# Performance work log

Hardware: AMD Instinct MI355X
Metric: run time of the kernel (lower is better)

The kernel has to match this reference:

```python
import jax, jax.numpy as jnp
import numpy as np

DILATED = (1, 2, 3)
NUM_PROTOS = 100
PROTO_SIZE = 4
ENC_SIZE = 1600
NUM_CLASSES = 2
B, L = 64, 256

# num_filters split exactly as in torch: floor(P/len) each, first gets remainder
_nf = [NUM_PROTOS // len(DILATED)] * len(DILATED)
_nf[0] += NUM_PROTOS % len(DILATED)
NUM_FILTERS = tuple(_nf)  # (34, 33, 33)


def setup_inputs() -> dict:
    key = jax.random.key(0)
    k1, k2, k3 = jax.random.split(key, 3)
    embedding = jax.random.normal(k1, (B, L, ENC_SIZE), dtype=jnp.float32)
    # nn.init.uniform_ default is U[0,1)
    protolayer = jax.random.uniform(k2, (NUM_PROTOS, ENC_SIZE, PROTO_SIZE), dtype=jnp.float32)
    fc_w = jax.random.normal(k3, (NUM_CLASSES, NUM_PROTOS), dtype=jnp.float32) * 0.1
    return {"embedding": embedding, "protolayer": protolayer, "fc_w": fc_w}


def _l2_convolution(x_bel, protolayer):
    # x_bel: [B, L, E] -> [B, E, L] for NCH conv layout
    x = jnp.transpose(x_bel, (0, 2, 1))
    # sliding-window sum of x^2 computed ONCE per dilation (shared across protos,
    # mathematically identical to conv1d with all-ones weight)
    s = jnp.sum(x * x, axis=1)  # [B, L]
    p2_sum = jnp.sum(protolayer * protolayer, axis=(1, 2))  # [P]
    distances = []
    j = 0
    Lx = x.shape[2]
    for d, n in zip(DILATED, NUM_FILTERS):
        L_out = Lx - (PROTO_SIZE - 1) * d
        # windowed sum over K=PROTO_SIZE taps with dilation d: [B, L_out]
        x2_patch = sum(s[:, k * d:k * d + L_out] for k in range(PROTO_SIZE))
        # dilated cross-correlation x * p : [B, n, L_out]
        xp = jax.lax.conv_general_dilated(
            x, protolayer[j:j + n],
            window_strides=(1,), padding='VALID', rhs_dilation=(d,),
            dimension_numbers=('NCH', 'OIH', 'NCH'))
        dist = jnp.sqrt(jnp.abs(x2_patch[:, None, :] - 2.0 * xp
                                + p2_sum[j:j + n][None, :, None]))
        distances.append(dist)
        j += n
    return distances


def reference(embedding, protolayer, fc_w):
    distances = _l2_convolution(embedding, protolayer)
    prototype_distances = jnp.concatenate(
        [jnp.min(d, axis=2) for d in distances], axis=1)  # [B, P]
    class_out = prototype_distances @ fc_w.T  # [B, num_classes]
    return (prototype_distances, distances[0], distances[1], distances[2], class_out)
```

## Files before the change

kernel.cpp:

```cpp
#include <hip/hip_runtime.h>

#define B_   64
#define L_   256
#define E_   1600
#define P_   100
#define KP   4
#define N0 34
#define N1 33
#define N2 33
#define LOUT0 253
#define LOUT1 250
#define LOUT2 247
#define OFF_PD 0
#define OFF_D0 6400
#define OFF_D1 (OFF_D0 + B_*N0*LOUT0)
#define OFF_D2 (OFF_D1 + B_*N1*LOUT1)
#define OFF_CO (OFF_D2 + B_*N2*LOUT2)

#define WS_ABF  0ull
#define WS_BT   52428800ull
#define WS_S    (WS_BT + 1280000ull)
#define WS_P2   (WS_S + 65536ull)
#define WS_NEED (WS_P2 + 512ull)

#define TMF  96
#define BKB  128
#define BOFF2 12288

typedef float f32x4 __attribute__((ext_vector_type(4)));
typedef unsigned short ushort8v __attribute__((ext_vector_type(8)));
typedef __bf16 bf16x8 __attribute__((ext_vector_type(8)));
typedef _Float16 f16;

__device__ __forceinline__ unsigned short bf16rne(float f) {
    unsigned u = __float_as_uint(f);
    u += 0x7FFFu + ((u >> 16) & 1u);
    return (unsigned short)(u >> 16);
}

typedef __attribute__((address_space(3))) void lds_void_t;
typedef __attribute__((address_space(1))) void glb_void_t;

__device__ __forceinline__ void gload16(const void* g, void* l) {
    __builtin_amdgcn_global_load_lds((const glb_void_t*)g, (lds_void_t*)l, 16, 0, 0);
}


__global__ __launch_bounds__(256) void proto_prep_fast(
        const float* __restrict__ emb, const float* __restrict__ proto,
        char* __restrict__ ws, float* __restrict__ out) {
    int q = blockIdx.x;
    int wave = threadIdx.x >> 6, lane = threadIdx.x & 63;
    if (q < 4096) {
        int row = q * 4 + wave;
        const float4* r = (const float4*)(emb + (size_t)row * E_);
        unsigned short* dst = (unsigned short*)(ws + WS_ABF + (size_t)row * (E_*2));
        float acc = 0.f;
        #pragma unroll
        for (int it = 0; it < 6; ++it) {
            int e4 = it * 64 + lane;
            float4 v = r[e4];
            acc += v.x*v.x + v.y*v.y + v.z*v.z + v.w*v.w;
            ushort4 bv = make_ushort4(bf16rne(v.x), bf16rne(v.y),
                                      bf16rne(v.z), bf16rne(v.w));
            *(ushort4*)(dst + e4 * 4) = bv;
        }
        if (lane < 16) {
            int e4 = 384 + lane;
            float4 v = r[e4];
            acc += v.x*v.x + v.y*v.y + v.z*v.z + v.w*v.w;
            ushort4 bv = make_ushort4(bf16rne(v.x), bf16rne(v.y),
                                      bf16rne(v.z), bf16rne(v.w));
            *(ushort4*)(dst + e4 * 4) = bv;
        }
        #pragma unroll
        for (int off = 32; off; off >>= 1) acc += __shfl_down(acc, off);
        if (lane == 0) ((float*)(ws + WS_S))[row] = acc;
    } else if (q < 4121) {
        int p = (q - 4096) * 4 + wave;
        if (p < P_) {
            const float4* r = (const float4*)(proto + (size_t)p * (E_ * KP));
            unsigned short* bt = (unsigned short*)(ws + WS_BT);
            float acc = 0.f;
            #pragma unroll
            for (int it = 0; it < 25; ++it) {
                int e = it * 64 + lane;
                float4 v = r[e];
                acc += v.x*v.x + v.y*v.y + v.z*v.z + v.w*v.w;
                bt[(size_t)(4*p + 0) * E_ + e] = bf16rne(v.x);
                bt[(size_t)(4*p + 1) * E_ + e] = bf16rne(v.y);
                bt[(size_t)(4*p + 2) * E_ + e] = bf16rne(v.z);
                bt[(size_t)(4*p + 3) * E_ + e] = bf16rne(v.w);
            }
            #pragma unroll
            for (int off = 32; off; off >>= 1) acc += __shfl_down(acc, off);
            if (lane == 0) ((float*)(ws + WS_P2))[p] = acc;
        }
    } else {
        for (int i = threadIdx.x; i < B_ * P_; i += 256)
            out[OFF_PD + i] = __uint_as_float(0x7F800000u);
    }
}

__global__ __launch_bounds__(192, 4) void proto_main_fast(
        const char* __restrict__ ws, float* __restrict__ out) {

    __shared__ __align__(16) char smem[22528];

    int bx   = blockIdx.x;
    int lb   = (bx & 7) * 120 + (bx >> 3);
    int b     = lb / 15;
    int inner = lb % 15;
    int m     = inner / 5;
    int n_blk = inner % 5;
    int r0    = (m == 0) ? 0 : (m == 1 ? 87 : 160);
    int l_lo  = m * 87;
    int pbase = n_blk * 20;

    const char* Ag = ws + WS_ABF + (size_t)(b * L_ + r0) * (E_ * 2);
    const char* Bg = ws + WS_BT  + (size_t)(pbase * 4) * (E_ * 2);

    int tid   = threadIdx.x;
    int lane  = tid & 63;
    int wave  = tid >> 6;
    int mrow  = lane & 15;
    int jq    = lane >> 4;
    int lrow8 = lane >> 3;
    int jst   = lane & 7;

    f32x4 acc[2][5] = {};

    for (int c = 0; c < 25; ++c) {
        int eoff = c * BKB;
        for (int t = wave; t < 22; t += 3) {
            if (t < 12) {
                int rowl = t * 8 + lrow8;
                int j = jst ^ (rowl & 7);
                gload16(Ag + (size_t)rowl * (E_*2) + eoff + j * 16,
                        smem + t * 1024);
            } else {
                int rowl = (t - 12) * 8 + lrow8;
                int j = jst ^ (rowl & 7);
                gload16(Bg + (size_t)rowl * (E_*2) + eoff + j * 16,
                        smem + BOFF2 + (t - 12) * 1024);
            }
        }
        __syncthreads();

        #pragma unroll
        for (int ks = 0; ks < 2; ++ks) {
            ushort8v af[2];
            #pragma unroll
            for (int mi = 0; mi < 2; ++mi) {
                int rowA = wave * 32 + mi * 16 + mrow;
                af[mi] = *(const ushort8v*)(smem + rowA * 128
                            + (((ks << 2) + jq) ^ (rowA & 7)) * 16);
            }
            ushort8v bfv[5];
            #pragma unroll
            for (int ni = 0; ni < 5; ++ni) {
                int rowB = ni * 16 + mrow;
                bfv[ni] = *(const ushort8v*)(smem + BOFF2 + rowB * 128
                            + (((ks << 2) + jq) ^ (rowB & 7)) * 16);
            }
            #pragma unroll
            for (int mi = 0; mi < 2; ++mi)
                #pragma unroll
                for (int ni = 0; ni < 5; ++ni)
                    acc[mi][ni] = __builtin_amdgcn_mfma_f32_16x16x32_bf16(
                        __builtin_bit_cast(bf16x8, af[mi]),
                        __builtin_bit_cast(bf16x8, bfv[ni]),
                        acc[mi][ni], 0, 0, 0);
        }
        __syncthreads();
    }

    f16*      Yh     = (f16*)smem;
    float*    slds   = (float*)(smem + 15552);
    float*    p2lds  = slds + TMF;
    unsigned* minlds = (unsigned*)(p2lds + 20);

    {
        int colq = lane & 15;
        int rowq = (lane >> 4) * 4;
        #pragma unroll
        for (int mi = 0; mi < 2; ++mi) {
            int row = wave * 32 + mi * 16 + rowq;
            #pragma unroll
            for (int ni = 0; ni < 5; ++ni) {
                int col = ni * 16 + colq;
                #pragma unroll
                for (int r = 0; r < 4; ++r)
                    Yh[(row + r) * 81 + col] = (f16)acc[mi][ni][r];
            }
        }
    }
    if (tid < TMF) slds[tid] = ((const float*)(ws + WS_S))[b * L_ + r0 + tid];
    if (tid < 20) {
        p2lds[tid] = ((const float*)(ws + WS_P2))[pbase + tid];
        minlds[tid] = 0x7F800000u;
    }
    __syncthreads();

    for (int idx = tid; idx < 20 * 87; idx += 192) {
        int pl  = idx / 87;
        int lof = idx % 87;
        int p = pbase + pl;
        int d, Lout, nseg, pseg; size_t segbase;
        if (p < 34)      { d = 1; Lout = LOUT0; segbase = OFF_D0; pseg = p;      nseg = N0; }
        else if (p < 67) { d = 2; Lout = LOUT1; segbase = OFF_D1; pseg = p - 34; nseg = N1; }
        else             { d = 3; Lout = LOUT2; segbase = OFF_D2; pseg = p - 67; nseg = N2; }
        int l = l_lo + lof;
        if (l < Lout) {
            int rl = l - r0;
            int c0 = pl * 4;
            float xp = (float)Yh[rl * 81 + c0]
                     + (float)Yh[(rl + d) * 81 + c0 + 1]
                     + (float)Yh[(rl + 2*d) * 81 + c0 + 2]
                     + (float)Yh[(rl + 3*d) * 81 + c0 + 3];
            float x2 = slds[rl] + slds[rl + d] + slds[rl + 2*d] + slds[rl + 3*d];
            float dist = sqrtf(fabsf(x2 - 2.f * xp + p2lds[pl]));
            out[segbase + ((size_t)b * nseg + pseg) * Lout + l] = dist;
            atomicMin(&minlds[pl], __float_as_uint(dist));
        }
    }
    __syncthreads();
    if (tid < 20)
        atomicMin((unsigned*)out + OFF_PD + b * P_ + pbase + tid, minlds[tid]);
}

#define TM   144
#define ASTR 40
#define YSTR 81

__global__ __launch_bounds__(256) void proto_prep_kernel(
        const float* __restrict__ emb, const float* __restrict__ proto,
        float* __restrict__ ws_s, float* __restrict__ ws_p2,
        float* __restrict__ out) {
    int q = blockIdx.x;
    int wave = threadIdx.x >> 6, lane = threadIdx.x & 63;
    if (q < 4096) {
        int row = q * 4 + wave;
        const float4* r = (const float4*)(emb + (size_t)row * E_);
        float acc = 0.f;
        #pragma unroll
        for (int it = 0; it < 7; ++it) {
            int e4 = it * 64 + lane;
            if (e4 < 400) {
                float4 v = r[e4];
                acc += v.x*v.x + v.y*v.y + v.z*v.z + v.w*v.w;
            }
        }
        #pragma unroll
        for (int off = 32; off; off >>= 1) acc += __shfl_down(acc, off);
        if (lane == 0) ws_s[row] = acc;
    } else if (q < 4121) {
        int p = (q - 4096) * 4 + wave;
        if (p < P_) {
            const float4* r = (const float4*)(proto + (size_t)p * (E_ * KP));
            float acc = 0.f;
            #pragma unroll
            for (int it = 0; it < 25; ++it) {
                float4 v = r[it * 64 + lane];
                acc += v.x*v.x + v.y*v.y + v.z*v.z + v.w*v.w;
            }
            #pragma unroll
            for (int off = 32; off; off >>= 1) acc += __shfl_down(acc, off);
            if (lane == 0) ws_p2[p] = acc;
        }
    } else {
        for (int i = threadIdx.x; i < B_ * P_; i += 256)
            out[OFF_PD + i] = __uint_as_float(0x7F800000u);
    }
}

__global__ __launch_bounds__(192) void proto_main_kernel(
        const float* __restrict__ emb, const float* __restrict__ proto,
        const float* __restrict__ ws_s, const float* __restrict__ ws_p2,
        float* __restrict__ out) {

    __shared__ __align__(16) char smem[47392];
    unsigned short* Ald = (unsigned short*)smem;
    unsigned short* Bld = (unsigned short*)(smem + TM*ASTR*2);

    int bx = blockIdx.x;
    int n_blk = bx % 5;
    int m     = (bx / 5) & 1;
    int b     = bx / 10;
    int r0    = m ? 112 : 0;
    int pbase = n_blk * 20;

    const float* Abase = emb + ((size_t)(b * L_ + r0)) * E_;
    const float* Bbase = proto + (size_t)pbase * (E_ * KP);

    int tid  = threadIdx.x;
    int lane = tid & 63;
    int wave = tid >> 6;
    int mrow = lane & 15;
    int kq   = (lane >> 4) * 8;

    f32x4 acc[3][5] = {};

    for (int c = 0; c < E_ / 32; ++c) {
        int e0 = c * 32;
        #pragma unroll
        for (int i = 0; i < 6; ++i) {
            int idx = tid + i * 192;
            int row = idx >> 3;
            int e4  = idx & 7;
            float4 v = *(const float4*)(Abase + (size_t)row * E_ + e0 + e4 * 4);
            ushort4 bv = make_ushort4(bf16rne(v.x), bf16rne(v.y),
                                      bf16rne(v.z), bf16rne(v.w));
            *(ushort4*)&Ald[row * ASTR + e4 * 4] = bv;
        }
        for (int idx = tid; idx < 640; idx += 192) {
            int pl = idx >> 5;
            int el = idx & 31;
            float4 v = *(const float4*)(Bbase + (size_t)pl * (E_ * KP)
                                        + (size_t)(e0 + el) * KP);
            Bld[(4*pl + 0) * ASTR + el] = bf16rne(v.x);
            Bld[(4*pl + 1) * ASTR + el] = bf16rne(v.y);
            Bld[(4*pl + 2) * ASTR + el] = bf16rne(v.z);
            Bld[(4*pl + 3) * ASTR + el] = bf16rne(v.w);
        }
        __syncthreads();

        ushort8v af[3], bfr[5];
        #pragma unroll
        for (int mi = 0; mi < 3; ++mi)
            af[mi] = *(const ushort8v*)&Ald[(wave*48 + mi*16 + mrow) * ASTR + kq];
        #pragma unroll
        for (int ni = 0; ni < 5; ++ni)
            bfr[ni] = *(const ushort8v*)&Bld[(ni*16 + mrow) * ASTR + kq];
        #pragma unroll
        for (int mi = 0; mi < 3; ++mi)
            #pragma unroll
            for (int ni = 0; ni < 5; ++ni)
                acc[mi][ni] = __builtin_amdgcn_mfma_f32_16x16x32_bf16(
                    __builtin_bit_cast(bf16x8, af[mi]),
                    __builtin_bit_cast(bf16x8, bfr[ni]),
                    acc[mi][ni], 0, 0, 0);
        __syncthreads();
    }

    float*    Ylds   = (float*)smem;
    float*    slds   = (float*)(smem + TM * YSTR * 4);
    float*    p2lds  = slds + TM;
    unsigned* minlds = (unsigned*)(p2lds + 20);

    {
        int colq = lane & 15;
        int rowq = (lane >> 4) * 4;
        #pragma unroll
        for (int mi = 0; mi < 3; ++mi) {
            int row = wave * 48 + mi * 16 + rowq;
            #pragma unroll
            for (int ni = 0; ni < 5; ++ni) {
                int col = ni * 16 + colq;
                #pragma unroll
                for (int r = 0; r < 4; ++r)
                    Ylds[(row + r) * YSTR + col] = acc[mi][ni][r];
            }
        }
    }
    if (tid < TM) slds[tid] = ws_s[b * L_ + r0 + tid];
    if (tid < 20) { p2lds[tid] = ws_p2[pbase + tid]; minlds[tid] = 0x7F800000u; }
    __syncthreads();

    int l_lo = m * 128;
    for (int idx = tid; idx < 20 * 128; idx += 192) {
        int pl  = idx >> 7;
        int lof = idx & 127;
        int p = pbase + pl;
        int d, Lout, nseg, pseg; size_t segbase;
        if (p < 34)      { d = 1; Lout = LOUT0; segbase = OFF_D0; pseg = p;      nseg = N0; }
        else if (p < 67) { d = 2; Lout = LOUT1; segbase = OFF_D1; pseg = p - 34; nseg = N1; }
        else             { d = 3; Lout = LOUT2; segbase = OFF_D2; pseg = p - 67; nseg = N2; }
        int l = l_lo + lof;
        if (l < Lout) {
            int rl = l - r0;
            int c0 = pl * 4;
            float xp = Ylds[rl * YSTR + c0]
                     + Ylds[(rl + d) * YSTR + c0 + 1]
                     + Ylds[(rl + 2*d) * YSTR + c0 + 2]
                     + Ylds[(rl + 3*d) * YSTR + c0 + 3];
            float x2 = slds[rl] + slds[rl + d] + slds[rl + 2*d] + slds[rl + 3*d];
            float dist = sqrtf(fabsf(x2 - 2.f * xp + p2lds[pl]));
            out[segbase + ((size_t)b * nseg + pseg) * Lout + l] = dist;
            atomicMin(&minlds[pl], __float_as_uint(dist));
        }
    }
    __syncthreads();
    if (tid < 20)
        atomicMin((unsigned*)out + OFF_PD + b * P_ + pbase + tid, minlds[tid]);
}

__global__ __launch_bounds__(128) void proto_fc_kernel(
        const float* __restrict__ fc_w, float* __restrict__ out) {
    int t = threadIdx.x;
    int b = t >> 1, c = t & 1;
    const float* pd = out + OFF_PD + b * P_;
    const float* w  = fc_w + c * P_;
    float s = 0.f;
    #pragma unroll 4
    for (int p = 0; p < P_; ++p) s += pd[p] * w[p];
    out[OFF_CO + b * 2 + c] = s;
}

extern "C" void kernel_launch(void* const* d_in, const int* in_sizes, int n_in,
                              void* d_out, int out_size, void* d_ws, size_t ws_size,
                              hipStream_t stream) {
    const float* emb   = (const float*)d_in[0];
    const float* proto = (const float*)d_in[1];
    const float* fc_w  = (const float*)d_in[2];
    float* out  = (float*)d_out;

    if (ws_size >= WS_NEED) {
        char* ws = (char*)d_ws;
        proto_prep_fast<<<4122, 256, 0, stream>>>(emb, proto, ws, out);
        proto_main_fast<<<960, 192, 0, stream>>>(ws, out);
    } else {
        float* ws_s  = (float*)d_ws;
        float* ws_p2 = ws_s + B_ * L_;
        proto_prep_kernel<<<4122, 256, 0, stream>>>(emb, proto, ws_s, ws_p2, out);
        proto_main_kernel<<<640, 192, 0, stream>>>(emb, proto, ws_s, ws_p2, out);
    }
    proto_fc_kernel<<<1, 128, 0, stream>>>(fc_w, out);
}
```

Measured before the change: 215.6 us.

## Fuse embedding bf16 conversion and squared-norm into main GEMM kernel

After: 236.0 us. +9.5%, slower.

```diff
diff --git a/kernel.cpp b/kernel.cpp
--- a/kernel.cpp
+++ b/kernel.cpp
@@ -17,14 +17,11 @@
 #define OFF_D2 (OFF_D1 + B_*N1*LOUT1)
 #define OFF_CO (OFF_D2 + B_*N2*LOUT2)
 
-#define WS_ABF  0ull
-#define WS_BT   52428800ull
-#define WS_S    (WS_BT + 1280000ull)
-#define WS_P2   (WS_S + 65536ull)
+#define WS_BT   0ull
+#define WS_P2   1280000ull
 #define WS_NEED (WS_P2 + 512ull)
 
 #define TMF  96
-#define BKB  128
 #define BOFF2 12288
 
 typedef float f32x4 __attribute__((ext_vector_type(4)));
@@ -46,64 +43,38 @@
 }
 
 
-__global__ __launch_bounds__(256) void proto_prep_fast(
-        const float* __restrict__ emb, const float* __restrict__ proto,
-        char* __restrict__ ws, float* __restrict__ out) {
+__global__ __launch_bounds__(256) void proto_prepB_fast(
+        const float* __restrict__ proto, char* __restrict__ ws,
+        float* __restrict__ out) {
     int q = blockIdx.x;
     int wave = threadIdx.x >> 6, lane = threadIdx.x & 63;
-    if (q < 4096) {
-        int row = q * 4 + wave;
-        const float4* r = (const float4*)(emb + (size_t)row * E_);
-        unsigned short* dst = (unsigned short*)(ws + WS_ABF + (size_t)row * (E_*2));
+    if (q < 25) {
+        int p = q * 4 + wave;
+        const float4* r = (const float4*)(proto + (size_t)p * (E_ * KP));
+        unsigned short* bt = (unsigned short*)(ws + WS_BT);
         float acc = 0.f;
         #pragma unroll
-        for (int it = 0; it < 6; ++it) {
-            int e4 = it * 64 + lane;
-            float4 v = r[e4];
+        for (int it = 0; it < 25; ++it) {
+            int e = it * 64 + lane;
+            float4 v = r[e];
             acc += v.x*v.x + v.y*v.y + v.z*v.z + v.w*v.w;
-            ushort4 bv = make_ushort4(bf16rne(v.x), bf16rne(v.y),
-                                      bf16rne(v.z), bf16rne(v.w));
-            *(ushort4*)(dst + e4 * 4) = bv;
-        }
-        if (lane < 16) {
-            int e4 = 384 + lane;
-            float4 v = r[e4];
-            acc += v.x*v.x + v.y*v.y + v.z*v.z + v.w*v.w;
-            ushort4 bv = make_ushort4(bf16rne(v.x), bf16rne(v.y),
-                                      bf16rne(v.z), bf16rne(v.w));
-            *(ushort4*)(dst + e4 * 4) = bv;
+            bt[(size_t)(4*p + 0) * E_ + e] = bf16rne(v.x);
+            bt[(size_t)(4*p + 1) * E_ + e] = bf16rne(v.y);
+            bt[(size_t)(4*p + 2) * E_ + e] = bf16rne(v.z);
+            bt[(size_t)(4*p + 3) * E_ + e] = bf16rne(v.w);
         }
         #pragma unroll
         for (int off = 32; off; off >>= 1) acc += __shfl_down(acc, off);
-        if (lane == 0) ((float*)(ws + WS_S))[row] = acc;
-    } else if (q < 4121) {
-        int p = (q - 4096) * 4 + wave;
-        if (p < P_) {
-            const float4* r = (const float4*)(proto + (size_t)p * (E_ * KP));
-            unsigned short* bt = (unsigned short*)(ws + WS_BT);
-            float acc = 0.f;
-            #pragma unroll
-            for (int it = 0; it < 25; ++it) {
-                int e = it * 64 + lane;
-                float4 v = r[e];
-                acc += v.x*v.x + v.y*v.y + v.z*v.z + v.w*v.w;
-                bt[(size_t)(4*p + 0) * E_ + e] = bf16rne(v.x);
-                bt[(size_t)(4*p + 1) * E_ + e] = bf16rne(v.y);
-                bt[(size_t)(4*p + 2) * E_ + e] = bf16rne(v.z);
-                bt[(size_t)(4*p + 3) * E_ + e] = bf16rne(v.w);
-            }
-            #pragma unroll
-            for (int off = 32; off; off >>= 1) acc += __shfl_down(acc, off);
-            if (lane == 0) ((float*)(ws + WS_P2))[p] = acc;
-        }
+        if (lane == 0) ((float*)(ws + WS_P2))[p] = acc;
     } else {
         for (int i = threadIdx.x; i < B_ * P_; i += 256)
             out[OFF_PD + i] = __uint_as_float(0x7F800000u);
     }
 }
 
-__global__ __launch_bounds__(192, 4) void proto_main_fast(
-        const char* __restrict__ ws, float* __restrict__ out) {
+__global__ __launch_bounds__(192, 3) void proto_main_fused(
+        const float* __restrict__ emb, const char* __restrict__ ws,
+        float* __restrict__ out) {
 
     __shared__ __align__(16) char smem[22528];
 
@@ -117,8 +88,8 @@
     int l_lo  = m * 87;
     int pbase = n_blk * 20;
 
-    const char* Ag = ws + WS_ABF + (size_t)(b * L_ + r0) * (E_ * 2);
-    const char* Bg = ws + WS_BT  + (size_t)(pbase * 4) * (E_ * 2);
+    const char* Ag = (const char*)emb + (size_t)(b * L_ + r0) * (E_ * 4);
+    const char* Bg = ws + WS_BT + (size_t)(pbase * 4) * (E_ * 2);
 
     int tid   = threadIdx.x;
     int lane  = tid & 63;
@@ -127,23 +98,38 @@
     int jq    = lane >> 4;
     int lrow8 = lane >> 3;
     int jst   = lane & 7;
+    int g8    = (tid >> 4) * 8;
+    int kk    = tid & 15;
 
     f32x4 acc[2][5] = {};
+    float sacc[8] = {};
 
     for (int c = 0; c < 25; ++c) {
-        int eoff = c * BKB;
-        for (int t = wave; t < 22; t += 3) {
-            if (t < 12) {
-                int rowl = t * 8 + lrow8;
-                int j = jst ^ (rowl & 7);
-                gload16(Ag + (size_t)rowl * (E_*2) + eoff + j * 16,
-                        smem + t * 1024);
-            } else {
-                int rowl = (t - 12) * 8 + lrow8;
-                int j = jst ^ (rowl & 7);
-                gload16(Bg + (size_t)rowl * (E_*2) + eoff + j * 16,
-                        smem + BOFF2 + (t - 12) * 1024);
-            }
+        int eoffB = c * 128;
+        int eoffA = c * 256;
+
+        for (int t = wave; t < 10; t += 3) {
+            int rowl = t * 8 + lrow8;
+            int j = jst ^ (rowl & 7);
+            gload16(Bg + (size_t)rowl * (E_*2) + eoffB + j * 16,
+                    smem + BOFF2 + t * 1024);
+        }
+
+        float4 va[8];
+        #pragma unroll
+        for (int i = 0; i < 8; ++i) {
+            int row = g8 + i;
+            va[i] = *(const float4*)(Ag + (size_t)row * (E_*4) + eoffA + kk * 16);
+        }
+        #pragma unroll
+        for (int i = 0; i < 8; ++i) {
+            int row = g8 + i;
+            float4 v = va[i];
+            sacc[i] += v.x*v.x + v.y*v.y + v.z*v.z + v.w*v.w;
+            ushort4 bv = make_ushort4(bf16rne(v.x), bf16rne(v.y),
+                                      bf16rne(v.z), bf16rne(v.w));
+            int gr = (kk >> 1) ^ (row & 7);
+            *(ushort4*)(smem + row * 128 + gr * 16 + (kk & 1) * 8) = bv;
         }
         __syncthreads();
 
@@ -177,8 +163,8 @@
 
     f16*      Yh     = (f16*)smem;
     float*    slds   = (float*)(smem + 15552);
-    float*    p2lds  = slds + TMF;
-    unsigned* minlds = (unsigned*)(p2lds + 20);
+    float*    p2lds  = (float*)(smem + 15936);
+    unsigned* minlds = (unsigned*)(smem + 16016);
 
     {
         int colq = lane & 15;
@@ -195,7 +181,19 @@
             }
         }
     }
-    if (tid < TMF) slds[tid] = ((const float*)(ws + WS_S))[b * L_ + r0 + tid];
+    #pragma unroll
+    for (int i = 0; i < 8; ++i) {
+        float v = sacc[i];
+        v += __shfl_xor(v, 1);
+        v += __shfl_xor(v, 2);
+        v += __shfl_xor(v, 4);
+        v += __shfl_xor(v, 8);
+        sacc[i] = v;
+    }
+    if (kk == 0) {
+        #pragma unroll
+        for (int i = 0; i < 8; ++i) slds[g8 + i] = sacc[i];
+    }
     if (tid < 20) {
         p2lds[tid] = ((const float*)(ws + WS_P2))[pbase + tid];
         minlds[tid] = 0x7F800000u;
@@ -417,8 +415,8 @@
 
     if (ws_size >= WS_NEED) {
         char* ws = (char*)d_ws;
-        proto_prep_fast<<<4122, 256, 0, stream>>>(emb, proto, ws, out);
-        proto_main_fast<<<960, 192, 0, stream>>>(ws, out);
+        proto_prepB_fast<<<26, 256, 0, stream>>>(proto, ws, out);
+        proto_main_fused<<<960, 192, 0, stream>>>(emb, ws, out);
     } else {
         float* ws_s  = (float*)d_ws;
         float* ws_p2 = ws_s + B_ * L_;
```
